# Optimization experiments

Measured on AMD Instinct MI355X. Metric: run time of the kernel, lower is better.

Reference implementation:

```python
import jax, jax.numpy as jnp
import numpy as np

B, N, M, D, H = 4, 1024, 1024, 1024, 16
HD = D // H
MH = int(D * 4.0 * 2 / 3)  # SwiGLU hidden = 2730
EPS = 1e-6


def setup_inputs() -> dict:
    key = jax.random.key(0)
    ks = jax.random.split(key, 16)
    w = lambda k, shape: jax.random.normal(k, shape, jnp.float32) * 0.02
    return dict(
        x=jax.random.normal(ks[0], (B, N, D), jnp.float32),
        source_tokens=jax.random.normal(ks[1], (B, M, D), jnp.float32),
        c=jax.random.normal(ks[2], (B, D), jnp.float32),
        ada_w=w(ks[3], (D, 9 * D)), ada_b=jnp.zeros((9 * D,), jnp.float32),
        n1_w=jnp.ones((D,), jnp.float32), nc_w=jnp.ones((D,), jnp.float32), n2_w=jnp.ones((D,), jnp.float32),
        sa_qkv_w=w(ks[4], (D, 3 * D)), sa_qkv_b=jnp.zeros((3 * D,), jnp.float32),
        sa_qn_w=jnp.ones((HD,), jnp.float32), sa_kn_w=jnp.ones((HD,), jnp.float32),
        sa_o_w=w(ks[5], (D, D)), sa_o_b=jnp.zeros((D,), jnp.float32),
        ca_q_w=w(ks[6], (D, D)), ca_q_b=jnp.zeros((D,), jnp.float32),
        ca_kv_w=w(ks[7], (D, 2 * D)), ca_kv_b=jnp.zeros((2 * D,), jnp.float32),
        ca_qn_w=jnp.ones((HD,), jnp.float32), ca_kn_w=jnp.ones((HD,), jnp.float32),
        ca_o_w=w(ks[8], (D, D)), ca_o_b=jnp.zeros((D,), jnp.float32),
        mlp_w1=w(ks[9], (D, MH)), mlp_b1=jnp.zeros((MH,), jnp.float32),
        mlp_w2=w(ks[10], (D, MH)), mlp_b2=jnp.zeros((MH,), jnp.float32),
        mlp_w3=w(ks[11], (MH, D)), mlp_b3=jnp.zeros((D,), jnp.float32),
    )


def _rms(x, w):
    return x * jax.lax.rsqrt(jnp.mean(x * x, axis=-1, keepdims=True) + EPS) * w


def _modulate(x, shift, scale):
    return x * (1.0 + scale[:, None, :]) + shift[:, None, :]


def _sdpa(q, k, v):
    # q: (B,Nq,H,HD), k/v: (B,Nk,H,HD)
    s = jnp.einsum('bqhd,bkhd->bhqk', q, k) * (HD ** -0.5)
    a = jax.nn.softmax(s, axis=-1)
    o = jnp.einsum('bhqk,bkhd->bqhd', a, v)
    return o.reshape(q.shape[0], q.shape[1], D)


def reference(x, source_tokens, c, ada_w, ada_b, n1_w, nc_w, n2_w,
              sa_qkv_w, sa_qkv_b, sa_qn_w, sa_kn_w, sa_o_w, sa_o_b,
              ca_q_w, ca_q_b, ca_kv_w, ca_kv_b, ca_qn_w, ca_kn_w, ca_o_w, ca_o_b,
              mlp_w1, mlp_b1, mlp_w2, mlp_b2, mlp_w3, mlp_b3):
    mods = jax.nn.silu(c) @ ada_w + ada_b
    (shift_sa, scale_sa, gate_sa, shift_ca, scale_ca, gate_ca,
     shift_ff, scale_ff, gate_ff) = jnp.split(mods, 9, axis=-1)

    # --- self-attention sublayer ---
    xn = _modulate(_rms(x, n1_w), shift_sa, scale_sa)
    qkv = xn @ sa_qkv_w + sa_qkv_b
    q, k, v = jnp.split(qkv, 3, axis=-1)
    q = _rms(q.reshape(B, N, H, HD), sa_qn_w)
    k = _rms(k.reshape(B, N, H, HD), sa_kn_w)
    v = v.reshape(B, N, H, HD)
    attn = _sdpa(q, k, v) @ sa_o_w + sa_o_b
    x = x + gate_sa[:, None, :] * attn

    # --- cross-attention sublayer ---
    xn = _modulate(_rms(x, nc_w), shift_ca, scale_ca)
    q = (xn @ ca_q_w + ca_q_b).reshape(B, N, H, HD)
    kv = source_tokens @ ca_kv_w + ca_kv_b
    k, v = jnp.split(kv, 2, axis=-1)
    q = _rms(q, ca_qn_w)
    k = _rms(k.reshape(B, M, H, HD), ca_kn_w)
    v = v.reshape(B, M, H, HD)
    cattn = _sdpa(q, k, v) @ ca_o_w + ca_o_b
    x = x + gate_ca[:, None, :] * cattn

    # --- SwiGLU FFN sublayer ---
    xn = _modulate(_rms(x, n2_w), shift_ff, scale_ff)
    ff = (jax.nn.silu(xn @ mlp_w1 + mlp_b1) * (xn @ mlp_w2 + mlp_b2)) @ mlp_w3 + mlp_b3
    x = x + gate_ff[:, None, :] * ff
    return x
```

## Files before the change

kernel.cpp:

```cpp
#include <hip/hip_runtime.h>

typedef unsigned short u16;
typedef __attribute__((ext_vector_type(8))) short short8;
typedef __attribute__((ext_vector_type(4))) float f32x4;

#define DD 1024
#define NN 1024
#define MODS_LD 9216

__device__ __forceinline__ float bf2f(u16 v) {
  unsigned int u = ((unsigned int)v) << 16;
  return __builtin_bit_cast(float, u);
}
__device__ __forceinline__ u16 f2bf(float f) {
  unsigned int u = __builtin_bit_cast(unsigned int, f);
  unsigned int lsb = (u >> 16) & 1;
  u += 0x7fffu + lsb;
  return (u16)(u >> 16);
}
__device__ __forceinline__ unsigned cvtpk_bf16(float a, float b) {
  unsigned r;
  asm volatile("v_cvt_pk_bf16_f32 %0, %1, %2" : "=v"(r) : "v"(a), "v"(b));
  return r;
}

__device__ __forceinline__ void gload_lds16(const u16* g, u16* l) {
  __builtin_amdgcn_global_load_lds(
      (const __attribute__((address_space(1))) unsigned int*)g,
      (__attribute__((address_space(3))) unsigned int*)l, 16, 0, 0);
}

__global__ void transpose_convert(const float* __restrict__ src, u16* __restrict__ dst,
                                  int R, int C, int R2, int C2) {
  __shared__ float tile[32][33];
  int tx = threadIdx.x, ty = threadIdx.y;
  int r0 = blockIdx.x * 32, c0 = blockIdx.y * 32;
#pragma unroll
  for (int i = 0; i < 4; ++i) {
    int r = r0 + ty + i * 8, c = c0 + tx;
    tile[ty + i * 8][tx] = (r < R && c < C) ? src[(long)r * C + c] : 0.f;
  }
  __syncthreads();
#pragma unroll
  for (int i = 0; i < 4; ++i) {
    int c = c0 + ty + i * 8, r = r0 + tx;
    if (c < C2 && r < R2) dst[(long)c * R2 + r] = f2bf(tile[tx][ty + i * 8]);
  }
}

__global__ void cvt_bf16_kernel(const float* __restrict__ in, u16* __restrict__ out, long n4) {
  long i = (long)blockIdx.x * 256 + threadIdx.x;
  if (i >= n4) return;
  float4 v = *(const float4*)&in[i * 4];
  ushort4 pk = {f2bf(v.x), f2bf(v.y), f2bf(v.z), f2bf(v.w)};
  *(ushort4*)&out[i * 4] = pk;
}

__global__ void silu_kernel(const float* __restrict__ c, float* __restrict__ sc) {
  int i = blockIdx.x * 256 + threadIdx.x;
  float v = c[i];
  sc[i] = v / (1.f + __expf(-v));
}

#define MODS_KS 32
__global__ __launch_bounds__(256) void mods_partial(const float* __restrict__ sc,
                                                    const float* __restrict__ aw,
                                                    float* __restrict__ part) {
  int j = blockIdx.x * 256 + threadIdx.x;
  int ks = blockIdx.y;
  int d0 = ks * (DD / MODS_KS);
  float a0 = 0.f, a1 = 0.f, a2 = 0.f, a3 = 0.f;
#pragma unroll 8
  for (int d = d0; d < d0 + DD / MODS_KS; ++d) {
    float w = aw[(long)d * MODS_LD + j];
    a0 = fmaf(sc[d], w, a0);
    a1 = fmaf(sc[DD + d], w, a1);
    a2 = fmaf(sc[2 * DD + d], w, a2);
    a3 = fmaf(sc[3 * DD + d], w, a3);
  }
  long base = (long)ks * 4 * MODS_LD + j;
  part[base] = a0;
  part[base + MODS_LD] = a1;
  part[base + 2 * MODS_LD] = a2;
  part[base + 3 * MODS_LD] = a3;
}

__global__ __launch_bounds__(256) void mods_reduce(const float* __restrict__ part,
                                                   const float* __restrict__ ab,
                                                   float* __restrict__ mods) {
  int j = blockIdx.x * 256 + threadIdx.x;
  int b = blockIdx.y;
  float acc = ab[j];
#pragma unroll
  for (int ks = 0; ks < MODS_KS; ++ks) acc += part[((long)ks * 4 + b) * MODS_LD + j];
  mods[(long)b * MODS_LD + j] = acc;
}

__global__ __launch_bounds__(256) void rmsmod_kernel(const float* __restrict__ x,
                                                     const float* __restrict__ w,
                                                     const float* __restrict__ mods,
                                                     int shiftOff, int scaleOff,
                                                     u16* __restrict__ out) {
  long row = blockIdx.x;
  int b = (int)(row >> 10);
  int t = threadIdx.x;
  const float* xr = x + row * DD;
  float4 v = *(const float4*)&xr[t * 4];
  float ss = v.x * v.x + v.y * v.y + v.z * v.z + v.w * v.w;
#pragma unroll
  for (int msk = 1; msk < 64; msk <<= 1) ss += __shfl_xor(ss, msk);
  __shared__ float red[4];
  if ((t & 63) == 0) red[t >> 6] = ss;
  __syncthreads();
  float tot = red[0] + red[1] + red[2] + red[3];
  float inv = rsqrtf(tot * (1.f / DD) + 1e-6f);
  const float* mrow = mods + (long)b * MODS_LD;
  float vv[4] = {v.x, v.y, v.z, v.w};
  u16 tmp[4];
#pragma unroll
  for (int j = 0; j < 4; ++j) {
    int c = t * 4 + j;
    float rr = vv[j] * inv * w[c] * (1.f + mrow[scaleOff + c]) + mrow[shiftOff + c];
    tmp[j] = f2bf(rr);
  }
  ushort4 pk = {tmp[0], tmp[1], tmp[2], tmp[3]};
  *(ushort4*)&out[row * DD + t * 4] = pk;
}

__global__ __launch_bounds__(256) void qknorm2_kernel(u16* __restrict__ bufq, int ldq,
                                                      const float* __restrict__ wq,
                                                      u16* __restrict__ bufk, int ldk,
                                                      const float* __restrict__ wk) {
  int which = blockIdx.y;
  u16* buf = which ? bufk : bufq;
  int ld = which ? ldk : ldq;
  const float* wgt = which ? wk : wq;
  float scale = which ? 1.0f : 0.125f;
  long row = blockIdx.x;
  int t = threadIdx.x;
  int g = t >> 4, p = t & 15;
  u16* ptr = buf + row * ld + g * 64 + p * 4;
  ushort4 a = *(ushort4*)ptr;
  float v[4] = {bf2f(a.x), bf2f(a.y), bf2f(a.z), bf2f(a.w)};
  float ss = v[0] * v[0] + v[1] * v[1] + v[2] * v[2] + v[3] * v[3];
  ss += __shfl_xor(ss, 1);
  ss += __shfl_xor(ss, 2);
  ss += __shfl_xor(ss, 4);
  ss += __shfl_xor(ss, 8);
  float inv = rsqrtf(ss * (1.f / 64) + 1e-6f) * scale;
  u16 o[4];
#pragma unroll
  for (int j = 0; j < 4; ++j) o[j] = f2bf(v[j] * inv * wgt[p * 4 + j]);
  ushort4 pk = {o[0], o[1], o[2], o[3]};
  *(ushort4*)ptr = pk;
}

__global__ void vtrans_kernel(const u16* __restrict__ vb, int kvStride, int Mpb,
                              u16* __restrict__ vt) {
  __shared__ u16 tile[64][66];
  int t = threadIdx.x;
  int kt = blockIdx.x, h = blockIdx.y, b = blockIdx.z;
  const u16* base = vb + ((long)(b * Mpb + kt * 64)) * kvStride + h * 64;
#pragma unroll
  for (int sh = 0; sh < 2; ++sh) {
    int r = sh * 32 + (t >> 3);
    int c0 = (t & 7) * 8;
    short8 vv = *(const short8*)(base + (long)r * kvStride + c0);
#pragma unroll
    for (int j = 0; j < 8; ++j) tile[c0 + j][r] = (u16)vv[j];
  }
  __syncthreads();
  u16* obase = vt + ((long)(b * 16 + h) * 64) * 1024 + kt * 64;
#pragma unroll
  for (int sh = 0; sh < 2; ++sh) {
    int d = sh * 32 + (t >> 3);
    int c0 = (t & 7) * 8;
    u16 tmp[8];
#pragma unroll
    for (int j = 0; j < 8; ++j) tmp[j] = tile[d][c0 + j];
    *(short8*)(obase + (long)d * 1024 + c0) = *(short8*)tmp;
  }
}

template <int MODE, int BN, int MINW>
__global__ __launch_bounds__(256, MINW) void gemm_bf16(
    const u16* __restrict__ A, const u16* __restrict__ Bt, int K, int ldc,
    const float* __restrict__ bias, int biasN, u16* __restrict__ outb,
    float* __restrict__ outf, const float* __restrict__ xin,
    const float* __restrict__ mods, int gateOff, int ncol) {
  constexpr int WC = BN / 2;
  constexpr int NT = WC / 16;
  constexpr int LOADS = 4 + BN / 32;
  __shared__ u16 As[2][128 * 64];
  __shared__ u16 Bs[2][BN * 64];
  int t = threadIdx.x;
  int l = t & 63, w = t >> 6;
  int wr = w >> 1, wc = w & 1;
  int lg = l >> 4, ll = l & 15;
  int rx = ll & 7;
  int nwg = gridDim.x, cpx = nwg >> 3, id = blockIdx.x;
  int wg = (id & 7) * cpx + (id >> 3);
  int tn = wg % ncol, tm = wg / ncol;
  long rowTile = (long)tm * 128;
  long colTile = (long)tn * BN;
  const u16* Ap = A + rowTile * K;
  const u16* Bp = Bt + colTile * K;
  int srow = t >> 3;
  int sck = ((t & 7) ^ (srow & 7)) * 8;

  auto stage = [&](int buf, int k0) {
#pragma unroll
    for (int i = 0; i < 4; ++i)
      gload_lds16(Ap + (long)(i * 32 + srow) * K + k0 + sck, &As[buf][(i * 256 + t) * 8]);
#pragma unroll
    for (int i = 0; i < BN / 32; ++i)
      gload_lds16(Bp + (long)(i * 32 + srow) * K + k0 + sck, &Bs[buf][(i * 256 + t) * 8]);
  };

  const int ntk = K >> 6;
  stage(0, 0);
  if (ntk > 1) stage(1, 64);

  f32x4 acc[4][NT] = {};
  int cur = 0;
  for (int i = 0; i < ntk; ++i) {
    if (i + 1 < ntk) {
      asm volatile("s_waitcnt vmcnt(%0)" ::"i"(LOADS) : "memory");
    } else {
      asm volatile("s_waitcnt vmcnt(0)" ::: "memory");
    }
    __builtin_amdgcn_s_barrier();
    const u16* Ac = As[cur];
    const u16* Bc = Bs[cur];
    short8 af[2][4], bfr[2][NT];
#pragma unroll
    for (int kk = 0; kk < 2; ++kk) {
#pragma unroll
      for (int m2 = 0; m2 < 4; ++m2)
        af[kk][m2] =
            *(const short8*)&Ac[(wr * 64 + m2 * 16 + ll) * 64 + (((kk * 4 + lg) ^ rx) << 3)];
#pragma unroll
      for (int n2 = 0; n2 < NT; ++n2)
        bfr[kk][n2] =
            *(const short8*)&Bc[(wc * WC + n2 * 16 + ll) * 64 + (((kk * 4 + lg) ^ rx) << 3)];
    }
    asm volatile("s_waitcnt lgkmcnt(0)" ::: "memory");
    __builtin_amdgcn_sched_barrier(0);
    __builtin_amdgcn_s_barrier();
    if (i + 2 < ntk) stage(cur, (i + 2) * 64);
    __builtin_amdgcn_s_setprio(1);
#pragma unroll
    for (int kk = 0; kk < 2; ++kk)
#pragma unroll
      for (int m2 = 0; m2 < 4; ++m2)
#pragma unroll
        for (int n2 = 0; n2 < NT; ++n2)
          acc[m2][n2] = __builtin_amdgcn_mfma_f32_16x16x32_bf16(af[kk][m2], bfr[kk][n2],
                                                                acc[m2][n2], 0, 0, 0);
    __builtin_amdgcn_s_setprio(0);
    cur ^= 1;
  }
#pragma unroll
  for (int n2 = 0; n2 < NT; ++n2) {
    long cg = colTile + wc * WC + n2 * 16 + ll;
    float bv = (cg < biasN) ? bias[cg] : 0.f;
#pragma unroll
    for (int m2 = 0; m2 < 4; ++m2) {
#pragma unroll
      for (int r = 0; r < 4; ++r) {
        long rg = rowTile + wr * 64 + m2 * 16 + lg * 4 + r;
        float v = acc[m2][n2][r] + bv;
        long idx = rg * ldc + cg;
        if (MODE == 0) {
          outb[idx] = f2bf(v);
        } else {
          int bb = (int)(rg >> 10);
          outf[idx] = xin[idx] + mods[(long)bb * MODS_LD + gateOff + cg] * v;
        }
      }
    }
  }
}

__global__ __launch_bounds__(256, 2) void gemm_dual_swiglu(
    const u16* __restrict__ A, const u16* __restrict__ B1t, const u16* __restrict__ B2t,
    int K, int ldc, const float* __restrict__ b1, const float* __restrict__ b2, int biasN,
    u16* __restrict__ outb, int ncol) {
  constexpr int BN = 64, WC = 32, NT = 2;
  __shared__ u16 As[2][128 * 64];
  __shared__ u16 B1s[2][BN * 64];
  __shared__ u16 B2s[2][BN * 64];
  int t = threadIdx.x;
  int l = t & 63, w = t >> 6;
  int wr = w >> 1, wc = w & 1;
  int lg = l >> 4, ll = l & 15;
  int rx = ll & 7;
  int nwg = gridDim.x, cpx = nwg >> 3, id = blockIdx.x;
  int wg = (id & 7) * cpx + (id >> 3);
  int tn = wg % ncol, tm = wg / ncol;
  long rowTile = (long)tm * 128;
  long colTile = (long)tn * BN;
  const u16* Ap = A + rowTile * K;
  const u16* B1p = B1t + colTile * K;
  const u16* B2p = B2t + colTile * K;
  int srow = t >> 3;
  int sck = ((t & 7) ^ (srow & 7)) * 8;

  auto stage = [&](int buf, int k0) {
#pragma unroll
    for (int i = 0; i < 4; ++i)
      gload_lds16(Ap + (long)(i * 32 + srow) * K + k0 + sck, &As[buf][(i * 256 + t) * 8]);
#pragma unroll
    for (int i = 0; i < 2; ++i) {
      gload_lds16(B1p + (long)(i * 32 + srow) * K + k0 + sck, &B1s[buf][(i * 256 + t) * 8]);
      gload_lds16(B2p + (long)(i * 32 + srow) * K + k0 + sck, &B2s[buf][(i * 256 + t) * 8]);
    }
  };

  const int ntk = K >> 6;
  stage(0, 0);
  if (ntk > 1) stage(1, 64);

  f32x4 acc1[4][NT] = {}, acc2[4][NT] = {};
  int cur = 0;
  for (int i = 0; i < ntk; ++i) {
    if (i + 1 < ntk) {
      asm volatile("s_waitcnt vmcnt(8)" ::: "memory");
    } else {
      asm volatile("s_waitcnt vmcnt(0)" ::: "memory");
    }
    __builtin_amdgcn_s_barrier();
    const u16* Ac = As[cur];
    const u16* B1c = B1s[cur];
    const u16* B2c = B2s[cur];
    short8 af[2][4], b1f[2][NT], b2f[2][NT];
#pragma unroll
    for (int kk = 0; kk < 2; ++kk) {
#pragma unroll
      for (int m2 = 0; m2 < 4; ++m2)
        af[kk][m2] =
            *(const short8*)&Ac[(wr * 64 + m2 * 16 + ll) * 64 + (((kk * 4 + lg) ^ rx) << 3)];
#pragma unroll
      for (int n2 = 0; n2 < NT; ++n2) {
        int off = (wc * WC + n2 * 16 + ll) * 64 + (((kk * 4 + lg) ^ rx) << 3);
        b1f[kk][n2] = *(const short8*)&B1c[off];
        b2f[kk][n2] = *(const short8*)&B2c[off];
      }
    }
    asm volatile("s_waitcnt lgkmcnt(0)" ::: "memory");
    __builtin_amdgcn_sched_barrier(0);
    __builtin_amdgcn_s_barrier();
    if (i + 2 < ntk) stage(cur, (i + 2) * 64);
    __builtin_amdgcn_s_setprio(1);
#pragma unroll
    for (int kk = 0; kk < 2; ++kk)
#pragma unroll
      for (int m2 = 0; m2 < 4; ++m2)
#pragma unroll
        for (int n2 = 0; n2 < NT; ++n2) {
          acc1[m2][n2] = __builtin_amdgcn_mfma_f32_16x16x32_bf16(af[kk][m2], b1f[kk][n2],
                                                                 acc1[m2][n2], 0, 0, 0);
          acc2[m2][n2] = __builtin_amdgcn_mfma_f32_16x16x32_bf16(af[kk][m2], b2f[kk][n2],
                                                                 acc2[m2][n2], 0, 0, 0);
        }
    __builtin_amdgcn_s_setprio(0);
    cur ^= 1;
  }
#pragma unroll
  for (int n2 = 0; n2 < NT; ++n2) {
    long cg = colTile + wc * WC + n2 * 16 + ll;
    float bv1 = (cg < biasN) ? b1[cg] : 0.f;
    float bv2 = (cg < biasN) ? b2[cg] : 0.f;
#pragma unroll
    for (int m2 = 0; m2 < 4; ++m2) {
#pragma unroll
      for (int r = 0; r < 4; ++r) {
        long rg = rowTile + wr * 64 + m2 * 16 + lg * 4 + r;
        float v1 = acc1[m2][n2][r] + bv1;
        float v2 = acc2[m2][n2][r] + bv2;
        float sg = v1 / (1.f + __expf(-v1));
        outb[rg * ldc + cg] = f2bf(sg * v2);
      }
    }
  }
}

__global__ __launch_bounds__(256, 3) void attn_kernel(
    const u16* __restrict__ qb, int qStride, const u16* __restrict__ kb, int kvStride,
    const u16* __restrict__ vt, u16* __restrict__ outp, int Nk, int Mpb) {
  __shared__ u16 Qs[64 * 64];
  __shared__ u16 Ks[2][64 * 64];
  __shared__ u16 Vs[2][64 * 64];
  __shared__ u16 Ps[4][16 * 64];
  int t = threadIdx.x, w = t >> 6, l = t & 63;
  int h = blockIdx.x, b = blockIdx.y, qt = blockIdx.z;
  int lg = l >> 4, ll = l & 15;
  int rx = ll & 7;

  const u16* Qbase = qb + ((long)(b * NN + qt * 64)) * qStride + h * 64;
  const u16* Kbase = kb + ((long)b * Mpb) * kvStride + h * 64;
  const u16* Vbase = vt + ((long)(b * 16 + h) * 64) * 1024;

  int srow = t >> 3;
  int schunk = t & 7;

#pragma unroll
  for (int sh = 0; sh < 2; ++sh) {
    int row = sh * 32 + srow;
    int ck = schunk ^ (row & 7);
    gload_lds16(Qbase + (long)row * qStride + ck * 8, &Qs[sh * 2048 + t * 8]);
  }
  auto stageKV = [&](int buf, int kt) {
    const u16* kn = Kbase + (long)kt * 64 * kvStride;
    const u16* vn = Vbase + kt * 64;
#pragma unroll
    for (int sh = 0; sh < 2; ++sh) {
      int row = sh * 32 + srow;
      int ck = schunk ^ (row & 7);
      gload_lds16(kn + (long)row * kvStride + ck * 8, &Ks[buf][sh * 2048 + t * 8]);
      gload_lds16(vn + (long)row * 1024 + ck * 8, &Vs[buf][sh * 2048 + t * 8]);
    }
  };
  const int ntk = Nk >> 6;
  stageKV(0, 0);
  if (ntk > 1) stageKV(1, 1);

  short8 qf0, qf1;
  float mrun = -1e30f, ssum = 0.f;
  f32x4 o[4] = {};

  int cur = 0;
  for (int kt = 0; kt < ntk; ++kt) {
    if (kt + 1 < ntk) {
      asm volatile("s_waitcnt vmcnt(4)" ::: "memory");
    } else {
      asm volatile("s_waitcnt vmcnt(0)" ::: "memory");
    }
    __builtin_amdgcn_s_barrier();
    if (kt == 0) {
      qf0 = *(const short8*)&Qs[(w * 16 + ll) * 64 + ((lg ^ rx) << 3)];
      qf1 = *(const short8*)&Qs[(w * 16 + ll) * 64 + (((4 + lg) ^ rx) << 3)];
    }
    const u16* Kc = Ks[cur];
    f32x4 s[4] = {};
#pragma unroll
    for (int n = 0; n < 4; ++n) {
      short8 kf0 = *(const short8*)&Kc[(n * 16 + ll) * 64 + ((lg ^ rx) << 3)];
      short8 kf1 = *(const short8*)&Kc[(n * 16 + ll) * 64 + (((4 + lg) ^ rx) << 3)];
      s[n] = __builtin_amdgcn_mfma_f32_16x16x32_bf16(kf0, qf0, s[n], 0, 0, 0);
      s[n] = __builtin_amdgcn_mfma_f32_16x16x32_bf16(kf1, qf1, s[n], 0, 0, 0);
    }
    float t0 = fmaxf(fmaxf(s[0][0], s[0][1]), fmaxf(s[0][2], s[0][3]));
    float t1 = fmaxf(fmaxf(s[1][0], s[1][1]), fmaxf(s[1][2], s[1][3]));
    float t2 = fmaxf(fmaxf(s[2][0], s[2][1]), fmaxf(s[2][2], s[2][3]));
    float t3 = fmaxf(fmaxf(s[3][0], s[3][1]), fmaxf(s[3][2], s[3][3]));
    float pm = fmaxf(fmaxf(t0, t1), fmaxf(t2, t3));
    pm = fmaxf(pm, __shfl_xor(pm, 16));
    pm = fmaxf(pm, __shfl_xor(pm, 32));
    float nm = fmaxf(mrun, pm);
    float alpha = __expf(mrun - nm);
    float pn[4][4];
#pragma unroll
    for (int n = 0; n < 4; ++n)
#pragma unroll
      for (int r = 0; r < 4; ++r) pn[n][r] = __expf(s[n][r] - nm);
    float r0 = (pn[0][0] + pn[0][1]) + (pn[0][2] + pn[0][3]);
    float r1 = (pn[1][0] + pn[1][1]) + (pn[1][2] + pn[1][3]);
    float r2 = (pn[2][0] + pn[2][1]) + (pn[2][2] + pn[2][3]);
    float r3 = (pn[3][0] + pn[3][1]) + (pn[3][2] + pn[3][3]);
    float rs = (r0 + r1) + (r2 + r3);
    rs += __shfl_xor(rs, 16);
    rs += __shfl_xor(rs, 32);
    ssum = ssum * alpha + rs;
    mrun = nm;
#pragma unroll
    for (int n = 0; n < 4; ++n) {
      uint2 pkd;
      pkd.x = cvtpk_bf16(pn[n][0], pn[n][1]);
      pkd.y = cvtpk_bf16(pn[n][2], pn[n][3]);
      int gran = n * 2 + (lg >> 1);
      int perm = gran ^ rx;
      *(uint2*)&Ps[w][ll * 64 + perm * 8 + (lg & 1) * 4] = pkd;
    }
    float a0 = __shfl(alpha, lg * 4 + 0);
    float a1 = __shfl(alpha, lg * 4 + 1);
    float a2 = __shfl(alpha, lg * 4 + 2);
    float a3 = __shfl(alpha, lg * 4 + 3);
#pragma unroll
    for (int n = 0; n < 4; ++n) {
      o[n][0] *= a0;
      o[n][1] *= a1;
      o[n][2] *= a2;
      o[n][3] *= a3;
    }
    short8 pf0 = *(const short8*)&Ps[w][ll * 64 + ((lg ^ rx) << 3)];
    short8 pf1 = *(const short8*)&Ps[w][ll * 64 + (((4 + lg) ^ rx) << 3)];
    const u16* Vc = Vs[cur];
    short8 vfr[4][2];
#pragma unroll
    for (int n = 0; n < 4; ++n) {
      vfr[n][0] = *(const short8*)&Vc[(n * 16 + ll) * 64 + ((lg ^ rx) << 3)];
      vfr[n][1] = *(const short8*)&Vc[(n * 16 + ll) * 64 + (((4 + lg) ^ rx) << 3)];
    }
    asm volatile("s_waitcnt lgkmcnt(0)" ::: "memory");
    __builtin_amdgcn_sched_barrier(0);
    __builtin_amdgcn_s_barrier();
    if (kt + 2 < ntk) stageKV(cur, kt + 2);
    __builtin_amdgcn_s_setprio(1);
#pragma unroll
    for (int n = 0; n < 4; ++n) {
      o[n] = __builtin_amdgcn_mfma_f32_16x16x32_bf16(pf0, vfr[n][0], o[n], 0, 0, 0);
      o[n] = __builtin_amdgcn_mfma_f32_16x16x32_bf16(pf1, vfr[n][1], o[n], 0, 0, 0);
    }
    __builtin_amdgcn_s_setprio(0);
    cur ^= 1;
  }
  float s0 = __shfl(ssum, lg * 4 + 0);
  float s1 = __shfl(ssum, lg * 4 + 1);
  float s2 = __shfl(ssum, lg * 4 + 2);
  float s3 = __shfl(ssum, lg * 4 + 3);
  float i0 = 1.f / s0, i1 = 1.f / s1, i2 = 1.f / s2, i3 = 1.f / s3;
#pragma unroll
  for (int n = 0; n < 4; ++n) {
    float ir[4] = {i0, i1, i2, i3};
#pragma unroll
    for (int r = 0; r < 4; ++r) {
      long row = (long)b * NN + qt * 64 + w * 16 + lg * 4 + r;
      int col = h * 64 + n * 16 + ll;
      outp[row * DD + col] = f2bf(o[n][r] * ir[r]);
    }
  }
}

extern "C" void kernel_launch(void* const* d_in, const int* in_sizes, int n_in,
                              void* d_out, int out_size, void* d_ws, size_t ws_size,
                              hipStream_t stream) {
  const float* x = (const float*)d_in[0];
  const float* src = (const float*)d_in[1];
  const float* c = (const float*)d_in[2];
  const float* ada_w = (const float*)d_in[3];
  const float* ada_b = (const float*)d_in[4];
  const float* n1_w = (const float*)d_in[5];
  const float* nc_w = (const float*)d_in[6];
  const float* n2_w = (const float*)d_in[7];
  const float* sa_qkv_w = (const float*)d_in[8];
  const float* sa_qkv_b = (const float*)d_in[9];
  const float* sa_qn_w = (const float*)d_in[10];
  const float* sa_kn_w = (const float*)d_in[11];
  const float* sa_o_w = (const float*)d_in[12];
  const float* sa_o_b = (const float*)d_in[13];
  const float* ca_q_w = (const float*)d_in[14];
  const float* ca_q_b = (const float*)d_in[15];
  const float* ca_kv_w = (const float*)d_in[16];
  const float* ca_kv_b = (const float*)d_in[17];
  const float* ca_qn_w = (const float*)d_in[18];
  const float* ca_kn_w = (const float*)d_in[19];
  const float* ca_o_w = (const float*)d_in[20];
  const float* ca_o_b = (const float*)d_in[21];
  const float* mlp_w1 = (const float*)d_in[22];
  const float* mlp_b1 = (const float*)d_in[23];
  const float* mlp_w2 = (const float*)d_in[24];
  const float* mlp_b2 = (const float*)d_in[25];
  const float* mlp_w3 = (const float*)d_in[26];
  const float* mlp_b3 = (const float*)d_in[27];
  float* out = (float*)d_out;

  char* p = (char*)d_ws;
  auto alloc = [&](size_t bytes) {
    char* r = p;
    p += (bytes + 255) & ~(size_t)255;
    return r;
  };
  float* mods = (float*)alloc(4l * 9216 * 4);
  float* sc = (float*)alloc(4096l * 4);
  float* part = (float*)alloc((long)MODS_KS * 4 * 9216 * 4);
  u16* qkvT = (u16*)alloc(3072l * 1024 * 2);
  u16* saoT = (u16*)alloc(1024l * 1024 * 2);
  u16* caqT = (u16*)alloc(1024l * 1024 * 2);
  u16* cakvT = (u16*)alloc(2048l * 1024 * 2);
  u16* caoT = (u16*)alloc(1024l * 1024 * 2);
  u16* w1T = (u16*)alloc(2816l * 1024 * 2);
  u16* w2T = (u16*)alloc(2816l * 1024 * 2);
  u16* w3T = (u16*)alloc(1024l * 2816 * 2);
  u16* xnb = (u16*)alloc(4096l * 1024 * 2);
  u16* srcb = (u16*)alloc(4096l * 1024 * 2);
  u16* bufA = (u16*)alloc(4096l * 3072 * 2);
  u16* bufB = (u16*)alloc(4096l * 2816 * 2);
  u16* attO = (u16*)alloc(4096l * 1024 * 2);
  u16* vtb = xnb;

  dim3 tb(32, 8);
  transpose_convert<<<dim3(32, 96), tb, 0, stream>>>(sa_qkv_w, qkvT, 1024, 3072, 1024, 3072);
  transpose_convert<<<dim3(32, 32), tb, 0, stream>>>(sa_o_w, saoT, 1024, 1024, 1024, 1024);
  transpose_convert<<<dim3(32, 32), tb, 0, stream>>>(ca_q_w, caqT, 1024, 1024, 1024, 1024);
  transpose_convert<<<dim3(32, 64), tb, 0, stream>>>(ca_kv_w, cakvT, 1024, 2048, 1024, 2048);
  transpose_convert<<<dim3(32, 32), tb, 0, stream>>>(ca_o_w, caoT, 1024, 1024, 1024, 1024);
  transpose_convert<<<dim3(32, 88), tb, 0, stream>>>(mlp_w1, w1T, 1024, 2730, 1024, 2816);
  transpose_convert<<<dim3(32, 88), tb, 0, stream>>>(mlp_w2, w2T, 1024, 2730, 1024, 2816);
  transpose_convert<<<dim3(88, 32), tb, 0, stream>>>(mlp_w3, w3T, 2730, 1024, 2816, 1024);
  cvt_bf16_kernel<<<4096, 256, 0, stream>>>(src, srcb, 4096l * 1024 / 4);
  silu_kernel<<<16, 256, 0, stream>>>(c, sc);
  mods_partial<<<dim3(36, MODS_KS), 256, 0, stream>>>(sc, ada_w, part);
  mods_reduce<<<dim3(36, 4), 256, 0, stream>>>(part, ada_b, mods);

  rmsmod_kernel<<<4096, 256, 0, stream>>>(x, n1_w, mods, 0, 1024, xnb);
  gemm_bf16<0, 128, 2><<<768, 256, 0, stream>>>(xnb, qkvT, 1024, 3072, sa_qkv_b, 3072, bufA,
                                                nullptr, nullptr, nullptr, 0, 24);
  qknorm2_kernel<<<dim3(4096, 2), 256, 0, stream>>>(bufA, 3072, sa_qn_w, bufA + 1024, 3072,
                                                    sa_kn_w);
  vtrans_kernel<<<dim3(16, 16, 4), 256, 0, stream>>>(bufA + 2048, 3072, 1024, vtb);
  attn_kernel<<<dim3(16, 4, 16), 256, 0, stream>>>(bufA, 3072, bufA + 1024, 3072, vtb, attO,
                                                   1024, 1024);
  gemm_bf16<1, 64, 3><<<512, 256, 0, stream>>>(attO, saoT, 1024, 1024, sa_o_b, 1024, nullptr,
                                               out, x, mods, 2048, 16);

  rmsmod_kernel<<<4096, 256, 0, stream>>>(out, nc_w, mods, 3072, 4096, xnb);
  gemm_bf16<0, 64, 3><<<512, 256, 0, stream>>>(xnb, caqT, 1024, 1024, ca_q_b, 1024, bufA,
                                               nullptr, nullptr, nullptr, 0, 16);
  gemm_bf16<0, 128, 2><<<512, 256, 0, stream>>>(srcb, cakvT, 1024, 2048, ca_kv_b, 2048, bufB,
                                                nullptr, nullptr, nullptr, 0, 16);
  qknorm2_kernel<<<dim3(4096, 2), 256, 0, stream>>>(bufA, 1024, ca_qn_w, bufB, 2048, ca_kn_w);
  vtrans_kernel<<<dim3(16, 16, 4), 256, 0, stream>>>(bufB + 1024, 2048, 1024, vtb);
  attn_kernel<<<dim3(16, 4, 16), 256, 0, stream>>>(bufA, 1024, bufB, 2048, vtb, attO, 1024,
                                                   1024);
  gemm_bf16<1, 64, 3><<<512, 256, 0, stream>>>(attO, caoT, 1024, 1024, ca_o_b, 1024, nullptr,
                                               out, out, mods, 5120, 16);

  rmsmod_kernel<<<4096, 256, 0, stream>>>(out, n2_w, mods, 6144, 7168, xnb);
  gemm_dual_swiglu<<<1408, 256, 0, stream>>>(xnb, w1T, w2T, 1024, 2816, mlp_b1, mlp_b2, 2730,
                                             bufA, 44);
  gemm_bf16<1, 64, 3><<<512, 256, 0, stream>>>(bufA, w3T, 2816, 1024, mlp_b3, 1024, nullptr,
                                               out, out, mods, 8192, 16);
}
```

Measured before the change: 384.5 us.

## Fuse QK RMS-norm into GEMM epilogue and attention, add XCD-aware tile mapping

Removes the standalone qknorm2 kernel. The K-head RMS norm now runs in the epilogue of the QKV/KV GEMMs, using a 16-lane shuffle reduction across each 64-column head. The Q norm, including the 1/8 softmax scale, is applied to the Q fragments when the attention kernel first loads them. A new xcd_tile mapping gives each XCD a rectangular chunk of output tiles to improve L2 reuse. This saves two launches and one bf16 read-write pass per attention, but adds epilogue branches and changes the work order.

```diff
diff --git a/kernel.cpp b/kernel.cpp
--- a/kernel.cpp
+++ b/kernel.cpp
@@ -28,6 +28,14 @@
   __builtin_amdgcn_global_load_lds(
       (const __attribute__((address_space(1))) unsigned int*)g,
       (__attribute__((address_space(3))) unsigned int*)l, 16, 0, 0);
+}
+
+__device__ __forceinline__ void xcd_tile(int ncolChunks, int cr, int cc, int& tm, int& tn) {
+  int id = blockIdx.x;
+  int c = id & 7, i = id >> 3;
+  int chunkRow = c / ncolChunks, chunkCol = c % ncolChunks;
+  tm = chunkRow * cr + (i % cr);
+  tn = chunkCol * cc + (i / cr);
 }
 
 __global__ void transpose_convert(const float* __restrict__ src, u16* __restrict__ dst,
@@ -127,34 +135,6 @@
   *(ushort4*)&out[row * DD + t * 4] = pk;
 }
 
-__global__ __launch_bounds__(256) void qknorm2_kernel(u16* __restrict__ bufq, int ldq,
-                                                      const float* __restrict__ wq,
-                                                      u16* __restrict__ bufk, int ldk,
-                                                      const float* __restrict__ wk) {
-  int which = blockIdx.y;
-  u16* buf = which ? bufk : bufq;
-  int ld = which ? ldk : ldq;
-  const float* wgt = which ? wk : wq;
-  float scale = which ? 1.0f : 0.125f;
-  long row = blockIdx.x;
-  int t = threadIdx.x;
-  int g = t >> 4, p = t & 15;
-  u16* ptr = buf + row * ld + g * 64 + p * 4;
-  ushort4 a = *(ushort4*)ptr;
-  float v[4] = {bf2f(a.x), bf2f(a.y), bf2f(a.z), bf2f(a.w)};
-  float ss = v[0] * v[0] + v[1] * v[1] + v[2] * v[2] + v[3] * v[3];
-  ss += __shfl_xor(ss, 1);
-  ss += __shfl_xor(ss, 2);
-  ss += __shfl_xor(ss, 4);
-  ss += __shfl_xor(ss, 8);
-  float inv = rsqrtf(ss * (1.f / 64) + 1e-6f) * scale;
-  u16 o[4];
-#pragma unroll
-  for (int j = 0; j < 4; ++j) o[j] = f2bf(v[j] * inv * wgt[p * 4 + j]);
-  ushort4 pk = {o[0], o[1], o[2], o[3]};
-  *(ushort4*)ptr = pk;
-}
-
 __global__ void vtrans_kernel(const u16* __restrict__ vb, int kvStride, int Mpb,
                               u16* __restrict__ vt) {
   __shared__ u16 tile[64][66];
@@ -182,12 +162,13 @@
   }
 }
 
-template <int MODE, int BN, int MINW>
+template <int MODE, int BN, int MINW, int NORM>
 __global__ __launch_bounds__(256, MINW) void gemm_bf16(
     const u16* __restrict__ A, const u16* __restrict__ Bt, int K, int ldc,
     const float* __restrict__ bias, int biasN, u16* __restrict__ outb,
     float* __restrict__ outf, const float* __restrict__ xin,
-    const float* __restrict__ mods, int gateOff, int ncol) {
+    const float* __restrict__ mods, int gateOff, int ncolChunks, int cr, int cc,
+    const float* __restrict__ nw, int normLo, int normHi, float nscale) {
   constexpr int WC = BN / 2;
   constexpr int NT = WC / 16;
   constexpr int LOADS = 4 + BN / 32;
@@ -198,9 +179,8 @@
   int wr = w >> 1, wc = w & 1;
   int lg = l >> 4, ll = l & 15;
   int rx = ll & 7;
-  int nwg = gridDim.x, cpx = nwg >> 3, id = blockIdx.x;
-  int wg = (id & 7) * cpx + (id >> 3);
-  int tn = wg % ncol, tm = wg / ncol;
+  int tm, tn;
+  xcd_tile(ncolChunks, cr, cc, tm, tn);
   long rowTile = (long)tm * 128;
   long colTile = (long)tn * BN;
   const u16* Ap = A + rowTile * K;
@@ -260,6 +240,42 @@
     __builtin_amdgcn_s_setprio(0);
     cur ^= 1;
   }
+
+  if (NORM == 1 && tn >= normLo && tn < normHi) {
+    float bv[NT], wnv[NT];
+#pragma unroll
+    for (int n2 = 0; n2 < NT; ++n2) {
+      long cg = colTile + wc * WC + n2 * 16 + ll;
+      bv[n2] = bias[cg];
+      wnv[n2] = nw[n2 * 16 + ll];
+    }
+#pragma unroll
+    for (int m2 = 0; m2 < 4; ++m2) {
+#pragma unroll
+      for (int r = 0; r < 4; ++r) {
+        float vals[NT];
+        float ss = 0.f;
+#pragma unroll
+        for (int n2 = 0; n2 < NT; ++n2) {
+          vals[n2] = acc[m2][n2][r] + bv[n2];
+          ss += vals[n2] * vals[n2];
+        }
+        ss += __shfl_xor(ss, 1);
+        ss += __shfl_xor(ss, 2);
+        ss += __shfl_xor(ss, 4);
+        ss += __shfl_xor(ss, 8);
+        float inv = rsqrtf(ss * (1.f / 64) + 1e-6f) * nscale;
+        long rg = rowTile + wr * 64 + m2 * 16 + lg * 4 + r;
+#pragma unroll
+        for (int n2 = 0; n2 < NT; ++n2) {
+          long cg = colTile + wc * WC + n2 * 16 + ll;
+          outb[rg * ldc + cg] = f2bf(vals[n2] * inv * wnv[n2]);
+        }
+      }
+    }
+    return;
+  }
+
 #pragma unroll
   for (int n2 = 0; n2 < NT; ++n2) {
     long cg = colTile + wc * WC + n2 * 16 + ll;
@@ -285,7 +301,7 @@
 __global__ __launch_bounds__(256, 2) void gemm_dual_swiglu(
     const u16* __restrict__ A, const u16* __restrict__ B1t, const u16* __restrict__ B2t,
     int K, int ldc, const float* __restrict__ b1, const float* __restrict__ b2, int biasN,
-    u16* __restrict__ outb, int ncol) {
+    u16* __restrict__ outb, int ncolChunks, int cr, int cc) {
   constexpr int BN = 64, WC = 32, NT = 2;
   __shared__ u16 As[2][128 * 64];
   __shared__ u16 B1s[2][BN * 64];
@@ -295,9 +311,8 @@
   int wr = w >> 1, wc = w & 1;
   int lg = l >> 4, ll = l & 15;
   int rx = ll & 7;
-  int nwg = gridDim.x, cpx = nwg >> 3, id = blockIdx.x;
-  int wg = (id & 7) * cpx + (id >> 3);
-  int tn = wg % ncol, tm = wg / ncol;
+  int tm, tn;
+  xcd_tile(ncolChunks, cr, cc, tm, tn);
   long rowTile = (long)tm * 128;
   long colTile = (long)tn * BN;
   const u16* Ap = A + rowTile * K;
@@ -387,7 +402,8 @@
 
 __global__ __launch_bounds__(256, 3) void attn_kernel(
     const u16* __restrict__ qb, int qStride, const u16* __restrict__ kb, int kvStride,
-    const u16* __restrict__ vt, u16* __restrict__ outp, int Nk, int Mpb) {
+    const u16* __restrict__ vt, const float* __restrict__ qn, u16* __restrict__ outp,
+    int Nk, int Mpb) {
   __shared__ u16 Qs[64 * 64];
   __shared__ u16 Ks[2][64 * 64];
   __shared__ u16 Vs[2][64 * 64];
@@ -440,6 +456,25 @@
     if (kt == 0) {
       qf0 = *(const short8*)&Qs[(w * 16 + ll) * 64 + ((lg ^ rx) << 3)];
       qf1 = *(const short8*)&Qs[(w * 16 + ll) * 64 + (((4 + lg) ^ rx) << 3)];
+      float qv0[8], qv1[8], ss = 0.f;
+#pragma unroll
+      for (int j = 0; j < 8; ++j) {
+        qv0[j] = bf2f((u16)qf0[j]);
+        qv1[j] = bf2f((u16)qf1[j]);
+        ss += qv0[j] * qv0[j] + qv1[j] * qv1[j];
+      }
+      ss += __shfl_xor(ss, 16);
+      ss += __shfl_xor(ss, 32);
+      float inv = rsqrtf(ss * (1.f / 64) + 1e-6f) * 0.125f;
+      int d0 = (lg ^ rx) << 3, d1 = ((4 + lg) ^ rx) << 3;
+      u16 t0[8], t1[8];
+#pragma unroll
+      for (int j = 0; j < 8; ++j) {
+        t0[j] = f2bf(qv0[j] * inv * qn[d0 + j]);
+        t1[j] = f2bf(qv1[j] * inv * qn[d1 + j]);
+      }
+      qf0 = *(short8*)t0;
+      qf1 = *(short8*)t1;
     }
     const u16* Kc = Ks[cur];
     f32x4 s[4] = {};
@@ -604,31 +639,34 @@
   mods_reduce<<<dim3(36, 4), 256, 0, stream>>>(part, ada_b, mods);
 
   rmsmod_kernel<<<4096, 256, 0, stream>>>(x, n1_w, mods, 0, 1024, xnb);
-  gemm_bf16<0, 128, 2><<<768, 256, 0, stream>>>(xnb, qkvT, 1024, 3072, sa_qkv_b, 3072, bufA,
-                                                nullptr, nullptr, nullptr, 0, 24);
-  qknorm2_kernel<<<dim3(4096, 2), 256, 0, stream>>>(bufA, 3072, sa_qn_w, bufA + 1024, 3072,
-                                                    sa_kn_w);
+  gemm_bf16<0, 128, 2, 1><<<768, 256, 0, stream>>>(xnb, qkvT, 1024, 3072, sa_qkv_b, 3072, bufA,
+                                                   nullptr, nullptr, nullptr, 0, 4, 16, 6,
+                                                   sa_kn_w, 8, 16, 1.0f);
   vtrans_kernel<<<dim3(16, 16, 4), 256, 0, stream>>>(bufA + 2048, 3072, 1024, vtb);
-  attn_kernel<<<dim3(16, 4, 16), 256, 0, stream>>>(bufA, 3072, bufA + 1024, 3072, vtb, attO,
+  attn_kernel<<<dim3(16, 4, 16), 256, 0, stream>>>(bufA, 3072, bufA + 1024, 3072, vtb, sa_qn_w,
+                                                   attO, 1024, 1024);
+  gemm_bf16<1, 64, 3, 0><<<512, 256, 0, stream>>>(attO, saoT, 1024, 1024, sa_o_b, 1024, nullptr,
+                                                  out, x, mods, 2048, 2, 8, 8, nullptr, 0, 0,
+                                                  0.f);
+
+  rmsmod_kernel<<<4096, 256, 0, stream>>>(out, nc_w, mods, 3072, 4096, xnb);
+  gemm_bf16<0, 64, 3, 0><<<512, 256, 0, stream>>>(xnb, caqT, 1024, 1024, ca_q_b, 1024, bufA,
+                                                  nullptr, nullptr, nullptr, 0, 2, 8, 8,
+                                                  nullptr, 0, 0, 0.f);
+  gemm_bf16<0, 128, 2, 1><<<512, 256, 0, stream>>>(srcb, cakvT, 1024, 2048, ca_kv_b, 2048, bufB,
+                                                   nullptr, nullptr, nullptr, 0, 2, 8, 8,
+                                                   ca_kn_w, 0, 8, 1.0f);
+  vtrans_kernel<<<dim3(16, 16, 4), 256, 0, stream>>>(bufB + 1024, 2048, 1024, vtb);
+  attn_kernel<<<dim3(16, 4, 16), 256, 0, stream>>>(bufA, 1024, bufB, 2048, vtb, ca_qn_w, attO,
                                                    1024, 1024);
-  gemm_bf16<1, 64, 3><<<512, 256, 0, stream>>>(attO, saoT, 1024, 1024, sa_o_b, 1024, nullptr,
-                                               out, x, mods, 2048, 16);
-
-  rmsmod_kernel<<<4096, 256, 0, stream>>>(out, nc_w, mods, 3072, 4096, xnb);
-  gemm_bf16<0, 64, 3><<<512, 256, 0, stream>>>(xnb, caqT, 1024, 1024, ca_q_b, 1024, bufA,
-                                               nullptr, nullptr, nullptr, 0, 16);
-  gemm_bf16<0, 128, 2><<<512, 256, 0, stream>>>(srcb, cakvT, 1024, 2048, ca_kv_b, 2048, bufB,
-                                                nullptr, nullptr, nullptr, 0, 16);
-  qknorm2_kernel<<<dim3(4096, 2), 256, 0, stream>>>(bufA, 1024, ca_qn_w, bufB, 2048, ca_kn_w);
-  vtrans_kernel<<<dim3(16, 16, 4), 256, 0, stream>>>(bufB + 1024, 2048, 1024, vtb);
-  attn_kernel<<<dim3(16, 4, 16), 256, 0, stream>>>(bufA, 1024, bufB, 2048, vtb, attO, 1024,
-                                                   1024);
-  gemm_bf16<1, 64, 3><<<512, 256, 0, stream>>>(attO, caoT, 1024, 1024, ca_o_b, 1024, nullptr,
-                                               out, out, mods, 5120, 16);
+  gemm_bf16<1, 64, 3, 0><<<512, 256, 0, stream>>>(attO, caoT, 1024, 1024, ca_o_b, 1024, nullptr,
+                                                  out, out, mods, 5120, 2, 8, 8, nullptr, 0, 0,
+                                                  0.f);
 
   rmsmod_kernel<<<4096, 256, 0, stream>>>(out, n2_w, mods, 6144, 7168, xnb);
   gemm_dual_swiglu<<<1408, 256, 0, stream>>>(xnb, w1T, w2T, 1024, 2816, mlp_b1, mlp_b2, 2730,
-                                             bufA, 44);
-  gemm_bf16<1, 64, 3><<<512, 256, 0, stream>>>(bufA, w3T, 2816, 1024, mlp_b3, 1024, nullptr,
-                                               out, out, mods, 8192, 16);
-}
+                                             bufA, 4, 16, 11);
+  gemm_bf16<1, 64, 3, 0><<<512, 256, 0, stream>>>(bufA, w3T, 2816, 1024, mlp_b3, 1024, nullptr,
+                                                  out, out, mods, 8192, 2, 8, 8, nullptr, 0, 0,
+                                                  0.f);
+}
```

After: 372.2 us. 3.2% less time.
